# Kernel tuning notes

Measured on AMD Instinct MI355X. Metric: run time of the kernel, lower is better.

Reference implementation:

```python
import jax, jax.numpy as jnp
import numpy as np

B, S, D = 2, 2048, 1024
E, H = 8, 2816  # hidden = 256*ceil(int(2*(4*1024)/3)/256) = 2816
TOP_K = 2


def setup_inputs() -> dict:
    key = jax.random.key(0)
    k0, k1, k2, k3, k4 = jax.random.split(key, 5)
    x = jax.random.normal(k0, (B, S, D), dtype=jnp.float32)
    wg = jax.random.normal(k1, (D, E), dtype=jnp.float32) * (D ** -0.5)
    w1 = jax.random.normal(k2, (E, D, H), dtype=jnp.float32) * 0.02  # gate proj
    w3 = jax.random.normal(k3, (E, D, H), dtype=jnp.float32) * 0.02  # up proj
    w2 = jax.random.normal(k4, (E, H, D), dtype=jnp.float32) * 0.02  # down proj
    return {"x": x, "wg": wg, "w1": w1, "w2": w2, "w3": w3}


def reference(x, wg, w1, w2, w3):
    Bb, Ss, Dd = x.shape
    Ee = w1.shape[0]
    xf = x.reshape(-1, Dd)                       # [T, D]
    logits = xf @ wg                              # [T, E]
    probs = jax.nn.softmax(logits, axis=-1)
    topk_p, topk_i = jax.lax.top_k(probs, TOP_K)  # [T, K]
    topk_p = topk_p / jnp.sum(topk_p, axis=-1, keepdims=True)
    # combine weight per (token, expert): sum over top-k slots
    cw = jnp.sum(jax.nn.one_hot(topk_i, Ee, dtype=xf.dtype) * topk_p[..., None], axis=1)  # [T, E]
    out = jnp.zeros_like(xf)
    for e in range(Ee):  # fixed small loop over experts
        h = jax.nn.silu(xf @ w1[e]) * (xf @ w3[e])   # [T, H] SwiGLU
        out = out + cw[:, e:e + 1] * (h @ w2[e])     # weighted combine
    return out.reshape(Bb, Ss, Dd)
```

## Files before the change

kernel.cpp:

```cpp
#include <hip/hip_runtime.h>
#include <hip/hip_bf16.h>

typedef unsigned short u16;
typedef __bf16 bf16_t;
typedef bf16_t bf16x8 __attribute__((ext_vector_type(8)));
typedef float f32x4 __attribute__((ext_vector_type(4)));

#define T_TOK 4096
#define DIM   1024
#define NEXP  8
#define HID   2816

static __device__ __forceinline__ u16 f2b(float f) {
    __hip_bfloat16 h = __float2bfloat16(f);
    return *(u16*)&h;
}

static __device__ __forceinline__ void glds16(const u16* g, u16* l) {
    __builtin_amdgcn_global_load_lds((const __attribute__((address_space(1))) void*)g,
                                     (__attribute__((address_space(3))) void*)l, 16, 0, 0);
}

__global__ void k_gating(const float* __restrict__ X,
                         const float* __restrict__ WG,
                         int* __restrict__ cnt,
                         int* __restrict__ tok,
                         float* __restrict__ wt)
{
    int wv   = threadIdx.x >> 6;
    int lane = threadIdx.x & 63;
    int t = blockIdx.x * 4 + wv;
    float l[NEXP];
#pragma unroll
    for (int e = 0; e < NEXP; ++e) l[e] = 0.f;
#pragma unroll
    for (int i = 0; i < DIM/64; ++i) {
        int d = i*64 + lane;
        float xv = X[(size_t)t*DIM + d];
        const float* wrow = WG + (size_t)d*NEXP;
        float4 wa = *(const float4*)wrow;
        float4 wb = *(const float4*)(wrow + 4);
        l[0] += xv*wa.x; l[1] += xv*wa.y; l[2] += xv*wa.z; l[3] += xv*wa.w;
        l[4] += xv*wb.x; l[5] += xv*wb.y; l[6] += xv*wb.z; l[7] += xv*wb.w;
    }
#pragma unroll
    for (int e = 0; e < NEXP; ++e) {
#pragma unroll
        for (int s = 32; s > 0; s >>= 1)
            l[e] += __shfl_xor(l[e], s, 64);
    }
    if (lane == 0) {
        int i1 = 0; float b1 = l[0];
#pragma unroll
        for (int e = 1; e < NEXP; ++e) if (l[e] > b1) { b1 = l[e]; i1 = e; }
        int i2 = -1; float b2 = 0.f;
#pragma unroll
        for (int e = 0; e < NEXP; ++e) {
            if (e == i1) continue;
            if (i2 < 0 || l[e] > b2) { b2 = l[e]; i2 = e; }
        }
        float p1 = 1.f / (1.f + __expf(b2 - b1));
        float p2 = 1.f - p1;
        int pos = atomicAdd(&cnt[i1], 1);
        tok[i1*T_TOK + pos] = t;  wt[i1*T_TOK + pos] = p1;
        pos = atomicAdd(&cnt[i2], 1);
        tok[i2*T_TOK + pos] = t;  wt[i2*T_TOK + pos] = p2;
    }
}

__global__ void k_compact(const int* __restrict__ cnt,
                          const int* __restrict__ tok, const float* __restrict__ wt,
                          int* __restrict__ ctok, float* __restrict__ cwt)
{
    int e = blockIdx.x;
    int off = 0;
    for (int i = 0; i < e; ++i) off += cnt[i];
    int n = cnt[e];
    for (int i = threadIdx.x; i < n; i += blockDim.x) {
        ctok[off + i] = tok[e*T_TOK + i];
        cwt [off + i] = wt [e*T_TOK + i];
    }
}

__global__ void k_transpose_cast(const float* __restrict__ in, u16* __restrict__ out,
                                 int R, int C)
{
    __shared__ u16 tle[64*72];
    size_t mb = (size_t)blockIdx.z * R * C;
    int r0 = blockIdx.x * 64, c0 = blockIdx.y * 64;
    int tid = threadIdx.x;
    for (int q = tid; q < 1024; q += 256) {
        int r = q >> 4, cc = (q & 15) * 4;
        float4 v = *(const float4*)&in[mb + (size_t)(r0+r)*C + c0 + cc];
        u16 b4[4] = { f2b(v.x), f2b(v.y), f2b(v.z), f2b(v.w) };
        *(uint2*)&tle[r*72 + cc] = *(const uint2*)b4;
    }
    __syncthreads();
    int hr = tid & 63;
    int dch = tid >> 6;
#pragma unroll
    for (int p = 0; p < 2; ++p) {
        int dc = dch + p*4;
        u16 v[8];
#pragma unroll
        for (int j = 0; j < 8; ++j) v[j] = tle[(dc*8 + j)*72 + hr];
        *(uint4*)&out[mb + (size_t)(c0+hr)*R + r0 + dc*8] = *(const uint4*)v;
    }
}

__global__ void k_castx(const float* __restrict__ in, u16* __restrict__ out)
{
    size_t i = ((size_t)blockIdx.x * 256 + threadIdx.x) * 8;
    float4 a = *(const float4*)&in[i];
    float4 b = *(const float4*)&in[i + 4];
    u16 v[8] = { f2b(a.x), f2b(a.y), f2b(a.z), f2b(a.w),
                 f2b(b.x), f2b(b.y), f2b(b.z), f2b(b.w) };
    *(uint4*)&out[i] = *(const uint4*)v;
}

__global__ __launch_bounds__(256) void k_gemm1(
    const u16* __restrict__ X, const u16* __restrict__ W1t, const u16* __restrict__ W3t,
    u16* __restrict__ Hbuf, const int* __restrict__ cnt, const int* __restrict__ ctok)
{
    __shared__ u16 As[128*32];
    __shared__ u16 Bs[128*32];
    __shared__ int tokLds[128];

    const int h0 = blockIdx.x * 64;
    const int e  = blockIdx.y;
    const int z  = blockIdx.z;

    int off = 0;
    for (int i = 0; i < e; ++i) off += cnt[i];
    const int ne = cnt[e];
    const int ntile = (ne + 127) >> 7;

    const int tid = threadIdx.x, wave = tid >> 6, lane = tid & 63;
    const int quad = lane >> 4, lr = lane & 15;
    const int lrow = lane >> 2;
    const int koff = (lane & 3) * 8;

    const size_t wbase = (size_t)e * HID * DIM;
    const u16* Wsel = (wave < 2) ? W1t : W3t;
    const int bcol0 = ((wave * 32) & 63) + lrow;
    const u16* bg0 = Wsel + wbase + (size_t)(h0 + bcol0)      * DIM + koff;
    const u16* bg1 = Wsel + wbase + (size_t)(h0 + bcol0 + 16) * DIM + koff;
    u16* al0 = &As[(wave*32)      * 32];
    u16* al1 = &As[(wave*32 + 16) * 32];
    u16* bl0 = &Bs[(wave*32)      * 32];
    u16* bl1 = &Bs[(wave*32 + 16) * 32];

    for (int mt = z; mt < ntile; mt += 2) {
        const int m0 = mt << 7;
        int nvalid = ne - m0; if (nvalid > 128) nvalid = 128;

        __syncthreads();
        if (tid < 128) {
            int i = (tid < nvalid) ? tid : (nvalid - 1);
            tokLds[tid] = ctok[off + m0 + i];
        }
        __syncthreads();
        const u16* ag0 = X + (size_t)tokLds[wave*32 + lrow]      * DIM + koff;
        const u16* ag1 = X + (size_t)tokLds[wave*32 + 16 + lrow] * DIM + koff;

        f32x4 acc1[2][4], acc3[2][4];
#pragma unroll
        for (int a = 0; a < 2; ++a)
#pragma unroll
            for (int b = 0; b < 4; ++b) {
                acc1[a][b] = (f32x4){0.f,0.f,0.f,0.f};
                acc3[a][b] = (f32x4){0.f,0.f,0.f,0.f};
            }

        for (int k0 = 0; k0 < DIM; k0 += 32) {
            __syncthreads();
            glds16(ag0 + k0, al0);
            glds16(ag1 + k0, al1);
            glds16(bg0 + k0, bl0);
            glds16(bg1 + k0, bl1);
            __syncthreads();
            bf16x8 af[2], b1[4], b3[4];
#pragma unroll
            for (int m = 0; m < 2; ++m)
                af[m] = *(const bf16x8*)&As[(wave*32 + m*16 + lr)*32 + quad*8];
#pragma unroll
            for (int n = 0; n < 4; ++n) {
                b1[n] = *(const bf16x8*)&Bs[(n*16 + lr)*32 + quad*8];
                b3[n] = *(const bf16x8*)&Bs[(64 + n*16 + lr)*32 + quad*8];
            }
#pragma unroll
            for (int m = 0; m < 2; ++m)
#pragma unroll
                for (int n = 0; n < 4; ++n) {
                    acc1[m][n] = __builtin_amdgcn_mfma_f32_16x16x32_bf16(af[m], b1[n], acc1[m][n], 0, 0, 0);
                    acc3[m][n] = __builtin_amdgcn_mfma_f32_16x16x32_bf16(af[m], b3[n], acc3[m][n], 0, 0, 0);
                }
        }

#pragma unroll
        for (int m = 0; m < 2; ++m) {
            int mb = wave*32 + m*16 + quad*4;
#pragma unroll
            for (int r = 0; r < 4; ++r) {
                int mm = mb + r;
                if (mm >= nvalid) continue;
                u16* hrow = Hbuf + (size_t)(off + m0 + mm)*HID + h0 + lr;
#pragma unroll
                for (int n = 0; n < 4; ++n) {
                    float g = acc1[m][n][r];
                    float u = acc3[m][n][r];
                    hrow[n*16] = f2b((g / (1.f + __expf(-g))) * u);
                }
            }
        }
    }
}

__global__ __launch_bounds__(256) void k_gemm2(
    const u16* __restrict__ Hbuf, const u16* __restrict__ W2t,
    float* __restrict__ outf, const int* __restrict__ cnt,
    const int* __restrict__ ctok, const float* __restrict__ cwt)
{
    __shared__ u16 As[128*32];
    __shared__ u16 Bs[128*32];
    __shared__ int   tLds[128];
    __shared__ float wLds[128];

    const int d0  = blockIdx.x * 128;
    const int e   = blockIdx.y;
    const int zmt = blockIdx.z >> 2;
    const int zk  = blockIdx.z & 3;
    const int kbase = zk * (HID/4);
    const int kend  = kbase + (HID/4);

    int off = 0;
    for (int i = 0; i < e; ++i) off += cnt[i];
    const int ne = cnt[e];
    const int ntile = (ne + 127) >> 7;

    const int tid = threadIdx.x, wave = tid >> 6, lane = tid & 63;
    const int quad = lane >> 4, lr = lane & 15;
    const int lrow = lane >> 2;
    const int koff = (lane & 3) * 8;

    const size_t w2base = (size_t)e * DIM * HID;
    const int bcol = wave*32 + lrow;
    const u16* bg0 = W2t + w2base + (size_t)(d0 + bcol)      * HID + koff;
    const u16* bg1 = W2t + w2base + (size_t)(d0 + bcol + 16) * HID + koff;
    u16* al0 = &As[(wave*32)      * 32];
    u16* al1 = &As[(wave*32 + 16) * 32];
    u16* bl0 = &Bs[(wave*32)      * 32];
    u16* bl1 = &Bs[(wave*32 + 16) * 32];

    for (int mt = zmt; mt < ntile; mt += 2) {
        const int m0 = mt << 7;
        int nvalid = ne - m0; if (nvalid > 128) nvalid = 128;

        __syncthreads();
        if (tid < 128) {
            int i = (tid < nvalid) ? tid : (nvalid - 1);
            tLds[tid] = ctok[off + m0 + i];
            wLds[tid] = cwt [off + m0 + i];
        }
        __syncthreads();
        int ar0 = wave*32 + lrow;       int ar0c = (ar0 < nvalid) ? ar0 : (nvalid - 1);
        int ar1 = ar0 + 16;             int ar1c = (ar1 < nvalid) ? ar1 : (nvalid - 1);
        const u16* ag0 = Hbuf + (size_t)(off + m0 + ar0c)*HID + koff;
        const u16* ag1 = Hbuf + (size_t)(off + m0 + ar1c)*HID + koff;

        f32x4 acc[2][8];
#pragma unroll
        for (int a = 0; a < 2; ++a)
#pragma unroll
            for (int b = 0; b < 8; ++b) acc[a][b] = (f32x4){0.f,0.f,0.f,0.f};

        for (int k0 = kbase; k0 < kend; k0 += 32) {
            __syncthreads();
            glds16(ag0 + k0, al0);
            glds16(ag1 + k0, al1);
            glds16(bg0 + k0, bl0);
            glds16(bg1 + k0, bl1);
            __syncthreads();
            bf16x8 af[2], bfr[8];
#pragma unroll
            for (int m = 0; m < 2; ++m)
                af[m] = *(const bf16x8*)&As[(wave*32 + m*16 + lr)*32 + quad*8];
#pragma unroll
            for (int n = 0; n < 8; ++n)
                bfr[n] = *(const bf16x8*)&Bs[(n*16 + lr)*32 + quad*8];
#pragma unroll
            for (int m = 0; m < 2; ++m)
#pragma unroll
                for (int n = 0; n < 8; ++n)
                    acc[m][n] = __builtin_amdgcn_mfma_f32_16x16x32_bf16(af[m], bfr[n], acc[m][n], 0, 0, 0);
        }

#pragma unroll
        for (int m = 0; m < 2; ++m) {
            int mb = wave*32 + m*16 + quad*4;
#pragma unroll
            for (int r = 0; r < 4; ++r) {
                int mm = mb + r;
                if (mm >= nvalid) continue;
                float wr = wLds[mm];
                float* orow = outf + (size_t)tLds[mm]*DIM + d0 + lr;
#pragma unroll
                for (int n = 0; n < 8; ++n)
                    atomicAdd(&orow[n*16], acc[m][n][r] * wr);
            }
        }
    }
}

extern "C" void kernel_launch(void* const* d_in, const int* in_sizes, int n_in,
                              void* d_out, int out_size, void* d_ws, size_t ws_size,
                              hipStream_t stream)
{
    const float* x  = (const float*)d_in[0];
    const float* wg = (const float*)d_in[1];
    const float* w1 = (const float*)d_in[2];
    const float* w2 = (const float*)d_in[3];
    const float* w3 = (const float*)d_in[4];
    float* outf = (float*)d_out;

    char* ws = (char*)d_ws;
    int*   cnt  = (int*)  (ws);
    int*   tok  = (int*)  (ws + 256);
    float* wt   = (float*)(ws + 131328);
    int*   ctok = (int*)  (ws + 262400);
    float* cwt  = (float*)(ws + 295168);
    u16*   Xbf  = (u16*)  (ws + 327936);
    u16*   Hbuf = (u16*)  (ws + 8716544);
    u16*   W1t  = (u16*)  (ws + 54853888);
    u16*   W3t  = (u16*)  (ws + 100991232);
    u16*   W2t  = (u16*)  (ws + 147128576);

    hipMemsetAsync(cnt, 0, 256, stream);
    hipMemsetAsync(outf, 0, (size_t)T_TOK*DIM*sizeof(float), stream);

    k_transpose_cast<<<dim3(DIM/64, HID/64, NEXP), 256, 0, stream>>>(w1, W1t, DIM, HID);
    k_transpose_cast<<<dim3(DIM/64, HID/64, NEXP), 256, 0, stream>>>(w3, W3t, DIM, HID);
    k_transpose_cast<<<dim3(HID/64, DIM/64, NEXP), 256, 0, stream>>>(w2, W2t, HID, DIM);
    k_castx<<<(T_TOK*DIM/8)/256, 256, 0, stream>>>(x, Xbf);

    k_gating<<<T_TOK/4, 256, 0, stream>>>(x, wg, cnt, tok, wt);
    k_compact<<<NEXP, 256, 0, stream>>>(cnt, tok, wt, ctok, cwt);

    k_gemm1<<<dim3(HID/64, NEXP, 2), 256, 0, stream>>>(Xbf, W1t, W3t, Hbuf, cnt, ctok);
    k_gemm2<<<dim3(DIM/128, NEXP, 8), 256, 0, stream>>>(Hbuf, W2t, outf, cnt, ctok, cwt);
}
```

Baseline: 740.1 us.

## Spread expert GEMM tiles over a flat grid, fuse x cast into gating

Both expert GEMMs move to a flat 1-D grid in which each block owns a single 128-token tile (up to CAP=16 per expert), and blocks with no tile exit early. This replaces the old scheme where two z-slices looped over all tiles serially, so far more blocks can run at once. The warp layout becomes 2x2 and gemm2's K split drops from 4 to 2, which halves the atomic adds into the output. The transpose kernel now transposes on the LDS write and does vectorised output stores, the separate x bf16 cast kernel is folded into gating, and launch bounds request 3 blocks per SM. The costs are many idle blocks that exit at once, and scalar LDS writes with possible bank conflicts in the transpose.

```diff
diff --git a/kernel.cpp b/kernel.cpp
--- a/kernel.cpp
+++ b/kernel.cpp
@@ -10,6 +10,7 @@
 #define DIM   1024
 #define NEXP  8
 #define HID   2816
+#define CAP   16
 
 static __device__ __forceinline__ u16 f2b(float f) {
     __hip_bfloat16 h = __float2bfloat16(f);
@@ -25,7 +26,8 @@
                          const float* __restrict__ WG,
                          int* __restrict__ cnt,
                          int* __restrict__ tok,
-                         float* __restrict__ wt)
+                         float* __restrict__ wt,
+                         u16* __restrict__ Xbf)
 {
     int wv   = threadIdx.x >> 6;
     int lane = threadIdx.x & 63;
@@ -37,6 +39,7 @@
     for (int i = 0; i < DIM/64; ++i) {
         int d = i*64 + lane;
         float xv = X[(size_t)t*DIM + d];
+        Xbf[(size_t)t*DIM + d] = f2b(xv);
         const float* wrow = WG + (size_t)d*NEXP;
         float4 wa = *(const float4*)wrow;
         float4 wb = *(const float4*)(wrow + 4);
@@ -82,43 +85,36 @@
     }
 }
 
+#define TS 72
 __global__ void k_transpose_cast(const float* __restrict__ in, u16* __restrict__ out,
                                  int R, int C)
 {
-    __shared__ u16 tle[64*72];
-    size_t mb = (size_t)blockIdx.z * R * C;
+    __shared__ u16 tle[64*TS];
+    size_t mb = (size_t)blockIdx.z * (size_t)R * C;
     int r0 = blockIdx.x * 64, c0 = blockIdx.y * 64;
     int tid = threadIdx.x;
-    for (int q = tid; q < 1024; q += 256) {
+    const float* I = in + mb + (size_t)r0*C + c0;
+#pragma unroll
+    for (int p = 0; p < 4; ++p) {
+        int q = tid + p*256;
         int r = q >> 4, cc = (q & 15) * 4;
-        float4 v = *(const float4*)&in[mb + (size_t)(r0+r)*C + c0 + cc];
-        u16 b4[4] = { f2b(v.x), f2b(v.y), f2b(v.z), f2b(v.w) };
-        *(uint2*)&tle[r*72 + cc] = *(const uint2*)b4;
+        float4 v = *(const float4*)&I[(size_t)r*C + cc];
+        tle[(cc+0)*TS + r] = f2b(v.x);
+        tle[(cc+1)*TS + r] = f2b(v.y);
+        tle[(cc+2)*TS + r] = f2b(v.z);
+        tle[(cc+3)*TS + r] = f2b(v.w);
     }
     __syncthreads();
-    int hr = tid & 63;
-    int dch = tid >> 6;
+    u16* O = out + mb + (size_t)c0*R + r0;
+    int rc = tid & 7, oc = tid >> 3;
 #pragma unroll
     for (int p = 0; p < 2; ++p) {
-        int dc = dch + p*4;
-        u16 v[8];
-#pragma unroll
-        for (int j = 0; j < 8; ++j) v[j] = tle[(dc*8 + j)*72 + hr];
-        *(uint4*)&out[mb + (size_t)(c0+hr)*R + r0 + dc*8] = *(const uint4*)v;
-    }
-}
-
-__global__ void k_castx(const float* __restrict__ in, u16* __restrict__ out)
-{
-    size_t i = ((size_t)blockIdx.x * 256 + threadIdx.x) * 8;
-    float4 a = *(const float4*)&in[i];
-    float4 b = *(const float4*)&in[i + 4];
-    u16 v[8] = { f2b(a.x), f2b(a.y), f2b(a.z), f2b(a.w),
-                 f2b(b.x), f2b(b.y), f2b(b.z), f2b(b.w) };
-    *(uint4*)&out[i] = *(const uint4*)v;
-}
-
-__global__ __launch_bounds__(256) void k_gemm1(
+        int c = oc + p*32;
+        *(uint4*)&O[(size_t)c*R + rc*8] = *(const uint4*)&tle[c*TS + rc*8];
+    }
+}
+
+__global__ __launch_bounds__(256, 3) void k_gemm1(
     const u16* __restrict__ X, const u16* __restrict__ W1t, const u16* __restrict__ W3t,
     u16* __restrict__ Hbuf, const int* __restrict__ cnt, const int* __restrict__ ctok)
 {
@@ -126,32 +122,33 @@
     __shared__ u16 Bs[128*32];
     __shared__ int tokLds[128];
 
-    const int h0 = blockIdx.x * 64;
-    const int e  = blockIdx.y;
-    const int z  = blockIdx.z;
-
+    const int bid = blockIdx.x;
+    const int e   = bid & 7;
+    const int q   = bid >> 3;
+    const int mt0 = q & (CAP-1);
+    const int col = q >> 4;
+    const int ne  = cnt[e];
+    const int ntile = (ne + 127) >> 7;
+    if (mt0 >= ntile) return;
     int off = 0;
     for (int i = 0; i < e; ++i) off += cnt[i];
-    const int ne = cnt[e];
-    const int ntile = (ne + 127) >> 7;
+    const int h0 = col * 64;
 
     const int tid = threadIdx.x, wave = tid >> 6, lane = tid & 63;
+    const int wr = wave >> 1, wc = wave & 1;
     const int quad = lane >> 4, lr = lane & 15;
-    const int lrow = lane >> 2;
-    const int koff = (lane & 3) * 8;
-
-    const size_t wbase = (size_t)e * HID * DIM;
-    const u16* Wsel = (wave < 2) ? W1t : W3t;
-    const int bcol0 = ((wave * 32) & 63) + lrow;
-    const u16* bg0 = Wsel + wbase + (size_t)(h0 + bcol0)      * DIM + koff;
-    const u16* bg1 = Wsel + wbase + (size_t)(h0 + bcol0 + 16) * DIM + koff;
-    u16* al0 = &As[(wave*32)      * 32];
-    u16* al1 = &As[(wave*32 + 16) * 32];
-    u16* bl0 = &Bs[(wave*32)      * 32];
-    u16* bl1 = &Bs[(wave*32 + 16) * 32];
-
-    for (int mt = z; mt < ntile; mt += 2) {
-        const int m0 = mt << 7;
+    const int lrow = lane >> 2, lko = (lane & 3) * 8;
+
+    const size_t wb = (size_t)e * HID * DIM;
+    const u16* w1g = W1t + wb + (size_t)(h0 + wave*16 + lrow)*DIM + lko;
+    const u16* w3g = W3t + wb + (size_t)(h0 + wave*16 + lrow)*DIM + lko;
+    u16* aL0 = &As[(wave*16)*32];
+    u16* aL1 = &As[(64 + wave*16)*32];
+    u16* bL0 = &Bs[(wave*16)*32];
+    u16* bL1 = &Bs[(64 + wave*16)*32];
+
+    for (int tile = mt0; tile < ntile; tile += CAP) {
+        const int m0 = tile << 7;
         int nvalid = ne - m0; if (nvalid > 128) nvalid = 128;
 
         __syncthreads();
@@ -160,55 +157,55 @@
             tokLds[tid] = ctok[off + m0 + i];
         }
         __syncthreads();
-        const u16* ag0 = X + (size_t)tokLds[wave*32 + lrow]      * DIM + koff;
-        const u16* ag1 = X + (size_t)tokLds[wave*32 + 16 + lrow] * DIM + koff;
-
-        f32x4 acc1[2][4], acc3[2][4];
-#pragma unroll
-        for (int a = 0; a < 2; ++a)
-#pragma unroll
-            for (int b = 0; b < 4; ++b) {
-                acc1[a][b] = (f32x4){0.f,0.f,0.f,0.f};
-                acc3[a][b] = (f32x4){0.f,0.f,0.f,0.f};
+        const u16* ag0 = X + (size_t)tokLds[wave*16 + lrow]*DIM + lko;
+        const u16* ag1 = X + (size_t)tokLds[64 + wave*16 + lrow]*DIM + lko;
+
+        f32x4 a1[4][2], a3[4][2];
+#pragma unroll
+        for (int m = 0; m < 4; ++m)
+#pragma unroll
+            for (int n = 0; n < 2; ++n) {
+                a1[m][n] = (f32x4){0.f,0.f,0.f,0.f};
+                a3[m][n] = (f32x4){0.f,0.f,0.f,0.f};
             }
 
         for (int k0 = 0; k0 < DIM; k0 += 32) {
             __syncthreads();
-            glds16(ag0 + k0, al0);
-            glds16(ag1 + k0, al1);
-            glds16(bg0 + k0, bl0);
-            glds16(bg1 + k0, bl1);
+            glds16(ag0 + k0, aL0);
+            glds16(ag1 + k0, aL1);
+            glds16(w1g + k0, bL0);
+            glds16(w3g + k0, bL1);
             __syncthreads();
-            bf16x8 af[2], b1[4], b3[4];
-#pragma unroll
-            for (int m = 0; m < 2; ++m)
-                af[m] = *(const bf16x8*)&As[(wave*32 + m*16 + lr)*32 + quad*8];
-#pragma unroll
-            for (int n = 0; n < 4; ++n) {
-                b1[n] = *(const bf16x8*)&Bs[(n*16 + lr)*32 + quad*8];
-                b3[n] = *(const bf16x8*)&Bs[(64 + n*16 + lr)*32 + quad*8];
+            bf16x8 af[4], b1[2], b3[2];
+#pragma unroll
+            for (int m = 0; m < 4; ++m)
+                af[m] = *(const bf16x8*)&As[(wr*64 + m*16 + lr)*32 + quad*8];
+#pragma unroll
+            for (int n = 0; n < 2; ++n) {
+                b1[n] = *(const bf16x8*)&Bs[(wc*32 + n*16 + lr)*32 + quad*8];
+                b3[n] = *(const bf16x8*)&Bs[(64 + wc*32 + n*16 + lr)*32 + quad*8];
             }
 #pragma unroll
-            for (int m = 0; m < 2; ++m)
-#pragma unroll
-                for (int n = 0; n < 4; ++n) {
-                    acc1[m][n] = __builtin_amdgcn_mfma_f32_16x16x32_bf16(af[m], b1[n], acc1[m][n], 0, 0, 0);
-                    acc3[m][n] = __builtin_amdgcn_mfma_f32_16x16x32_bf16(af[m], b3[n], acc3[m][n], 0, 0, 0);
+            for (int m = 0; m < 4; ++m)
+#pragma unroll
+                for (int n = 0; n < 2; ++n) {
+                    a1[m][n] = __builtin_amdgcn_mfma_f32_16x16x32_bf16(af[m], b1[n], a1[m][n], 0, 0, 0);
+                    a3[m][n] = __builtin_amdgcn_mfma_f32_16x16x32_bf16(af[m], b3[n], a3[m][n], 0, 0, 0);
                 }
         }
 
 #pragma unroll
-        for (int m = 0; m < 2; ++m) {
-            int mb = wave*32 + m*16 + quad*4;
-#pragma unroll
-            for (int r = 0; r < 4; ++r) {
-                int mm = mb + r;
+        for (int m = 0; m < 4; ++m) {
+            int mb_ = wr*64 + m*16 + quad*4;
+#pragma unroll
+            for (int rr = 0; rr < 4; ++rr) {
+                int mm = mb_ + rr;
                 if (mm >= nvalid) continue;
-                u16* hrow = Hbuf + (size_t)(off + m0 + mm)*HID + h0 + lr;
-#pragma unroll
-                for (int n = 0; n < 4; ++n) {
-                    float g = acc1[m][n][r];
-                    float u = acc3[m][n][r];
+                u16* hrow = Hbuf + (size_t)(off + m0 + mm)*HID + h0 + wc*32 + lr;
+#pragma unroll
+                for (int n = 0; n < 2; ++n) {
+                    float g = a1[m][n][rr];
+                    float u = a3[m][n][rr];
                     hrow[n*16] = f2b((g / (1.f + __expf(-g))) * u);
                 }
             }
@@ -216,7 +213,7 @@
     }
 }
 
-__global__ __launch_bounds__(256) void k_gemm2(
+__global__ __launch_bounds__(256, 3) void k_gemm2(
     const u16* __restrict__ Hbuf, const u16* __restrict__ W2t,
     float* __restrict__ outf, const int* __restrict__ cnt,
     const int* __restrict__ ctok, const float* __restrict__ cwt)
@@ -226,34 +223,35 @@
     __shared__ int   tLds[128];
     __shared__ float wLds[128];
 
-    const int d0  = blockIdx.x * 128;
-    const int e   = blockIdx.y;
-    const int zmt = blockIdx.z >> 2;
-    const int zk  = blockIdx.z & 3;
-    const int kbase = zk * (HID/4);
-    const int kend  = kbase + (HID/4);
-
+    const int bid = blockIdx.x;
+    const int e   = bid & 7;
+    const int q   = bid >> 3;
+    const int mt0 = q & (CAP-1);
+    const int r2  = q >> 4;
+    const int zk  = r2 & 1;
+    const int d0  = (r2 >> 1) * 128;
+    const int ne  = cnt[e];
+    const int ntile = (ne + 127) >> 7;
+    if (mt0 >= ntile) return;
     int off = 0;
     for (int i = 0; i < e; ++i) off += cnt[i];
-    const int ne = cnt[e];
-    const int ntile = (ne + 127) >> 7;
+    const int kb = zk * (HID/2);
 
     const int tid = threadIdx.x, wave = tid >> 6, lane = tid & 63;
+    const int wr = wave >> 1, wc = wave & 1;
     const int quad = lane >> 4, lr = lane & 15;
-    const int lrow = lane >> 2;
-    const int koff = (lane & 3) * 8;
-
-    const size_t w2base = (size_t)e * DIM * HID;
-    const int bcol = wave*32 + lrow;
-    const u16* bg0 = W2t + w2base + (size_t)(d0 + bcol)      * HID + koff;
-    const u16* bg1 = W2t + w2base + (size_t)(d0 + bcol + 16) * HID + koff;
-    u16* al0 = &As[(wave*32)      * 32];
-    u16* al1 = &As[(wave*32 + 16) * 32];
-    u16* bl0 = &Bs[(wave*32)      * 32];
-    u16* bl1 = &Bs[(wave*32 + 16) * 32];
-
-    for (int mt = zmt; mt < ntile; mt += 2) {
-        const int m0 = mt << 7;
+    const int lrow = lane >> 2, lko = (lane & 3) * 8;
+
+    const size_t w2b = (size_t)e * DIM * HID;
+    const u16* bg0 = W2t + w2b + (size_t)(d0 + wave*16 + lrow)*HID + kb + lko;
+    const u16* bg1 = bg0 + (size_t)64*HID;
+    u16* aL0 = &As[(wave*16)*32];
+    u16* aL1 = &As[(64 + wave*16)*32];
+    u16* bL0 = &Bs[(wave*16)*32];
+    u16* bL1 = &Bs[(64 + wave*16)*32];
+
+    for (int tile = mt0; tile < ntile; tile += CAP) {
+        const int m0 = tile << 7;
         int nvalid = ne - m0; if (nvalid > 128) nvalid = 128;
 
         __syncthreads();
@@ -263,50 +261,50 @@
             wLds[tid] = cwt [off + m0 + i];
         }
         __syncthreads();
-        int ar0 = wave*32 + lrow;       int ar0c = (ar0 < nvalid) ? ar0 : (nvalid - 1);
-        int ar1 = ar0 + 16;             int ar1c = (ar1 < nvalid) ? ar1 : (nvalid - 1);
-        const u16* ag0 = Hbuf + (size_t)(off + m0 + ar0c)*HID + koff;
-        const u16* ag1 = Hbuf + (size_t)(off + m0 + ar1c)*HID + koff;
-
-        f32x4 acc[2][8];
-#pragma unroll
-        for (int a = 0; a < 2; ++a)
-#pragma unroll
-            for (int b = 0; b < 8; ++b) acc[a][b] = (f32x4){0.f,0.f,0.f,0.f};
-
-        for (int k0 = kbase; k0 < kend; k0 += 32) {
+        int ar0 = wave*16 + lrow;      if (ar0 >= nvalid) ar0 = nvalid - 1;
+        int ar1 = 64 + wave*16 + lrow; if (ar1 >= nvalid) ar1 = nvalid - 1;
+        const u16* ag0 = Hbuf + (size_t)(off + m0 + ar0)*HID + kb + lko;
+        const u16* ag1 = Hbuf + (size_t)(off + m0 + ar1)*HID + kb + lko;
+
+        f32x4 acc[4][4];
+#pragma unroll
+        for (int a = 0; a < 4; ++a)
+#pragma unroll
+            for (int b = 0; b < 4; ++b) acc[a][b] = (f32x4){0.f,0.f,0.f,0.f};
+
+        for (int k0 = 0; k0 < HID/2; k0 += 32) {
             __syncthreads();
-            glds16(ag0 + k0, al0);
-            glds16(ag1 + k0, al1);
-            glds16(bg0 + k0, bl0);
-            glds16(bg1 + k0, bl1);
+            glds16(ag0 + k0, aL0);
+            glds16(ag1 + k0, aL1);
+            glds16(bg0 + k0, bL0);
+            glds16(bg1 + k0, bL1);
             __syncthreads();
-            bf16x8 af[2], bfr[8];
-#pragma unroll
-            for (int m = 0; m < 2; ++m)
-                af[m] = *(const bf16x8*)&As[(wave*32 + m*16 + lr)*32 + quad*8];
-#pragma unroll
-            for (int n = 0; n < 8; ++n)
-                bfr[n] = *(const bf16x8*)&Bs[(n*16 + lr)*32 + quad*8];
-#pragma unroll
-            for (int m = 0; m < 2; ++m)
-#pragma unroll
-                for (int n = 0; n < 8; ++n)
-                    acc[m][n] = __builtin_amdgcn_mfma_f32_16x16x32_bf16(af[m], bfr[n], acc[m][n], 0, 0, 0);
-        }
-
-#pragma unroll
-        for (int m = 0; m < 2; ++m) {
-            int mb = wave*32 + m*16 + quad*4;
-#pragma unroll
-            for (int r = 0; r < 4; ++r) {
-                int mm = mb + r;
+            bf16x8 af[4], bf[4];
+#pragma unroll
+            for (int m = 0; m < 4; ++m)
+                af[m] = *(const bf16x8*)&As[(wr*64 + m*16 + lr)*32 + quad*8];
+#pragma unroll
+            for (int n = 0; n < 4; ++n)
+                bf[n] = *(const bf16x8*)&Bs[(wc*64 + n*16 + lr)*32 + quad*8];
+#pragma unroll
+            for (int m = 0; m < 4; ++m)
+#pragma unroll
+                for (int n = 0; n < 4; ++n)
+                    acc[m][n] = __builtin_amdgcn_mfma_f32_16x16x32_bf16(af[m], bf[n], acc[m][n], 0, 0, 0);
+        }
+
+#pragma unroll
+        for (int m = 0; m < 4; ++m) {
+            int mb_ = wr*64 + m*16 + quad*4;
+#pragma unroll
+            for (int rr = 0; rr < 4; ++rr) {
+                int mm = mb_ + rr;
                 if (mm >= nvalid) continue;
-                float wr = wLds[mm];
-                float* orow = outf + (size_t)tLds[mm]*DIM + d0 + lr;
-#pragma unroll
-                for (int n = 0; n < 8; ++n)
-                    atomicAdd(&orow[n*16], acc[m][n][r] * wr);
+                float wr_ = wLds[mm];
+                float* orow = outf + (size_t)tLds[mm]*DIM + d0 + wc*64 + lr;
+#pragma unroll
+                for (int n = 0; n < 4; ++n)
+                    atomicAdd(&orow[n*16], acc[m][n][rr] * wr_);
             }
         }
     }
@@ -341,11 +339,10 @@
     k_transpose_cast<<<dim3(DIM/64, HID/64, NEXP), 256, 0, stream>>>(w1, W1t, DIM, HID);
     k_transpose_cast<<<dim3(DIM/64, HID/64, NEXP), 256, 0, stream>>>(w3, W3t, DIM, HID);
     k_transpose_cast<<<dim3(HID/64, DIM/64, NEXP), 256, 0, stream>>>(w2, W2t, HID, DIM);
-    k_castx<<<(T_TOK*DIM/8)/256, 256, 0, stream>>>(x, Xbf);
-
-    k_gating<<<T_TOK/4, 256, 0, stream>>>(x, wg, cnt, tok, wt);
+
+    k_gating<<<T_TOK/4, 256, 0, stream>>>(x, wg, cnt, tok, wt, Xbf);
     k_compact<<<NEXP, 256, 0, stream>>>(cnt, tok, wt, ctok, cwt);
 
-    k_gemm1<<<dim3(HID/64, NEXP, 2), 256, 0, stream>>>(Xbf, W1t, W3t, Hbuf, cnt, ctok);
-    k_gemm2<<<dim3(DIM/128, NEXP, 8), 256, 0, stream>>>(Hbuf, W2t, outf, cnt, ctok, cwt);
-}
+    k_gemm1<<<NEXP*(HID/64)*CAP, 256, 0, stream>>>(Xbf, W1t, W3t, Hbuf, cnt, ctok);
+    k_gemm2<<<NEXP*CAP*2*(DIM/128), 256, 0, stream>>>(Hbuf, W2t, outf, cnt, ctok, cwt);
+}
```

After: 671.6 us. 1.1x faster.
